# Performance work log

Hardware: AMD Instinct MI355X
Metric: run time of the kernel (lower is better)

The kernel has to match this reference:

```python
import jax, jax.numpy as jnp
import numpy as np
from jax import lax

D_STATE, D_ADAPT, D_CNN, D_RNN, D_OUT, HORIZON = 12, 16, 64, 256, 2, 10
B, L, H, W = 32, 16, 112, 112
DN = ('NCHW', 'OIHW', 'NCHW')
BN_EPS = 1e-5


def setup_inputs() -> dict:
    key = jax.random.key(0)
    ks = jax.random.split(key, 22)
    rn = lambda k, shape, s=0.05: jax.random.normal(k, shape, jnp.float32) * s
    return {
        'x': jax.random.normal(ks[0], (B, L, D_STATE), jnp.float32),
        'frames': jax.random.normal(ks[1], (B, L, 3, H, W), jnp.float32),
        # backbone `cnn`: 16x16 stride-16 patchify conv 3 -> 576 (gives 7x7 spatial)
        'cnn_w': rn(ks[2], (576, 3, 16, 16)), 'cnn_b': rn(ks[3], (576,)),
        # cnn_1: Conv2d(576, 64, 3, padding=1) + ReLU + BatchNorm (eval) + Dropout (eval=identity)
        'cnn1_w': rn(ks[4], (D_CNN, 576, 3, 3)), 'cnn1_b': rn(ks[5], (D_CNN,)),
        'bn_g': jnp.ones((D_CNN,), jnp.float32), 'bn_b': jnp.zeros((D_CNN,), jnp.float32),
        'bn_m': jnp.zeros((D_CNN,), jnp.float32), 'bn_v': jnp.ones((D_CNN,), jnp.float32),
        'a0_w': rn(ks[6], (D_ADAPT, D_STATE)), 'a0_b': rn(ks[7], (D_ADAPT,)),
        'ai_w': rn(ks[8], (D_ADAPT, D_ADAPT)), 'ai_b': rn(ks[9], (D_ADAPT,)),
        'an_w': rn(ks[10], (D_RNN, D_CNN + D_ADAPT)), 'an_b': rn(ks[11], (D_RNN,)),
        # single-layer batch_first GRU, PyTorch gate layout [r, z, n]
        'w_ih': rn(ks[12], (3 * D_RNN, D_RNN)), 'w_hh': rn(ks[13], (3 * D_RNN, D_RNN)),
        'b_ih': rn(ks[14], (3 * D_RNN,)), 'b_hh': rn(ks[15], (3 * D_RNN,)),
        'fi_w': rn(ks[16], (D_RNN, D_RNN)), 'fi_b': rn(ks[17], (D_RNN,)),
        'fn_w': rn(ks[18], (D_OUT, D_RNN)), 'fn_b': rn(ks[19], (D_OUT,)),
    }


def _gru_cell(xt, h, w_ih, w_hh, b_ih, b_hh):
    gi = xt @ w_ih.T + b_ih  # (B, 3*D)
    gh = h @ w_hh.T + b_hh
    i_r, i_z, i_n = jnp.split(gi, 3, axis=-1)
    h_r, h_z, h_n = jnp.split(gh, 3, axis=-1)
    r = jax.nn.sigmoid(i_r + h_r)
    z = jax.nn.sigmoid(i_z + h_z)
    n = jnp.tanh(i_n + r * h_n)
    return (1.0 - z) * n + z * h


def _forward(x, frames, cnn_w, cnn_b, cnn1_w, cnn1_b, bn_g, bn_b, bn_m, bn_v,
             a0_w, a0_b, ai_w, ai_b, an_w, an_b, w_ih, w_hh, b_ih, b_hh,
             fi_w, fi_b, fn_w, fn_b):
    b, l = frames.shape[0], frames.shape[1]
    f = frames.reshape((-1,) + frames.shape[-3:])  # (b*l, 3, H, W)
    # backbone cnn: patchify conv -> (b*l, 576, 7, 7)
    f = lax.conv_general_dilated(f, cnn_w, (16, 16), 'VALID', dimension_numbers=DN) + cnn_b[:, None, None]
    # cnn_1: Conv3x3 same -> ReLU -> BatchNorm(eval) -> Dropout(eval=identity)
    f = lax.conv_general_dilated(f, cnn1_w, (1, 1), 'SAME', dimension_numbers=DN) + cnn1_b[:, None, None]
    f = jax.nn.relu(f)
    inv = bn_g / jnp.sqrt(bn_v + BN_EPS)
    f = (f - bn_m[:, None, None]) * inv[:, None, None] + bn_b[:, None, None]
    # AdaptiveAvgPool2d((1,1)) then reshape to (b, l, d_cnn)
    f = f.mean(axis=(2, 3)).reshape(b, l, -1)
    # state adapters
    s = jax.nn.relu(x @ a0_w.T + a0_b)
    s = s + jax.nn.relu(s @ ai_w.T + ai_b)
    s = jnp.concatenate([s, f], axis=-1)  # (b, l, d_cnn + d_adapt)
    s = jax.nn.relu(s @ an_w.T + an_b)    # (b, l, d_rnn)
    # encoder GRU over the l frames
    d_rnn = w_hh.shape[1]
    h0 = jnp.zeros((b, d_rnn), s.dtype)
    def enc_step(h, xt):
        h2 = _gru_cell(xt, h, w_ih, w_hh, b_ih, b_hh)
        return h2, None
    h, _ = lax.scan(enc_step, h0, jnp.swapaxes(s, 0, 1))
    x_in = h  # last output of single-layer GRU == final hidden state
    def dec_step(carry, _):
        xi, hh = carry
        hn = _gru_cell(xi, hh, w_ih, w_hh, b_ih, b_hh)  # one GRU step; output == new hidden
        xr = hn + jax.nn.relu(hn @ fi_w.T + fi_b)       # final_i residual
        pred = jnp.tanh(xr @ fn_w.T + fn_b)             # final_n head
        return (xr, hn), pred
    _, preds = lax.scan(dec_step, (x_in, h), None, length=HORIZON)
    return preds[:, :, None, :]  # (horizon, b, 1, d_out) matching torch.stack of (b,1,d_out)


def reference(x, frames, cnn_w, cnn_b, cnn1_w, cnn1_b, bn_g, bn_b, bn_m, bn_v,
              a0_w, a0_b, ai_w, ai_b, an_w, an_b, w_ih, w_hh, b_ih, b_hh,
              fi_w, fi_b, fn_w, fn_b):
    return _forward(x, frames, cnn_w, cnn_b, cnn1_w, cnn1_b, bn_g, bn_b, bn_m, bn_v,
                    a0_w, a0_b, ai_w, ai_b, an_w, an_b, w_ih, w_hh, b_ih, b_hh,
                    fi_w, fi_b, fn_w, fn_b)
```

## Files before the change

kernel.cpp:

```cpp
#include <hip/hip_runtime.h>

typedef unsigned short u16;
typedef unsigned int u32;
typedef __bf16 bf16x8 __attribute__((ext_vector_type(8)));
typedef float f32x4 __attribute__((ext_vector_type(4)));
typedef unsigned short u16x8 __attribute__((ext_vector_type(8)));
typedef unsigned int u32x4 __attribute__((ext_vector_type(4)));
typedef _Float16 v2h __attribute__((ext_vector_type(2)));

__device__ __forceinline__ u16 f2bf(float f) {
    unsigned u = __float_as_uint(f);
    u = (u + 0x7fffu + ((u >> 16) & 1u)) >> 16;
    return (u16)u;
}
__device__ __forceinline__ float bf2f(u16 h) {
    return __uint_as_float((unsigned)h << 16);
}
__device__ __forceinline__ u32 packh2(float a, float b) {
    _Float16 ha = (_Float16)a, hb = (_Float16)b;
    u16 la = __builtin_bit_cast(u16, ha), lb = __builtin_bit_cast(u16, hb);
    return (u32)la | ((u32)lb << 16);
}
__device__ __forceinline__ float dot2acc(u32 w, u32 h, float acc) {
#if __has_builtin(__builtin_amdgcn_fdot2)
    return __builtin_amdgcn_fdot2(__builtin_bit_cast(v2h, w),
                                  __builtin_bit_cast(v2h, h), acc, false);
#else
    v2h wv = __builtin_bit_cast(v2h, w), hv = __builtin_bit_cast(v2h, h);
    return acc + (float)wv.x * (float)hv.x + (float)wv.y * (float)hv.y;
#endif
}
__device__ __forceinline__ float dot8(u32x4 w, u32x4 h, float acc) {
    acc = dot2acc(w.x, h.x, acc);
    acc = dot2acc(w.y, h.y, acc);
    acc = dot2acc(w.z, h.z, acc);
    acc = dot2acc(w.w, h.w, acc);
    return acc;
}
__device__ __forceinline__ void gload_lds16(const void* g, void* l) {
    __builtin_amdgcn_global_load_lds(
        (const __attribute__((address_space(1))) unsigned int*)g,
        (__attribute__((address_space(3))) unsigned int*)l, 16, 0, 0);
}

__global__ __launch_bounds__(256) void prep_kernel(
    const float* __restrict__ cnn_w, const float* __restrict__ cnn1_w,
    const float* __restrict__ w_hh, const float* __restrict__ w_ih,
    const float* __restrict__ fi_w,
    u16* __restrict__ B1, u16* __restrict__ B2,
    u32* __restrict__ whh8, u32* __restrict__ wih8, u32* __restrict__ fi8,
    u32* __restrict__ zpage)
{
    int idx = blockIdx.x * 256 + threadIdx.x;
    if (idx < 442368) { B1[idx] = f2bf(cnn_w[idx]); return; }
    idx -= 442368;
    if (idx < 331776) {
        int n = idx / 5184, rem = idx - n * 5184;
        int off = rem / 576, c = rem - off * 576;
        int dy = off / 3, dx = off - dy * 3;
        B2[idx] = f2bf(cnn1_w[((n * 576 + c) * 3 + dy) * 3 + dx]);
        return;
    }
    idx -= 331776;
    if (idx < 98304) {
        int kb = idx / 3072, r = idx - kb * 3072;
        int o = r >> 2, c = r & 3;
        int kk = kb * 8 + c * 2;
        whh8[idx] = packh2(w_hh[o * 256 + kk], w_hh[o * 256 + kk + 1]);
        return;
    }
    idx -= 98304;
    if (idx < 98304) {
        int kb = idx / 3072, r = idx - kb * 3072;
        int o = r >> 2, c = r & 3;
        int kk = kb * 8 + c * 2;
        wih8[idx] = packh2(w_ih[o * 256 + kk], w_ih[o * 256 + kk + 1]);
        return;
    }
    idx -= 98304;
    if (idx < 32768) {
        int kb = idx / 1024, r = idx - kb * 1024;
        int u = r >> 2, c = r & 3;
        int kk = kb * 8 + c * 2;
        fi8[idx] = packh2(fi_w[u * 256 + kk], fi_w[u * 256 + kk + 1]);
        return;
    }
    idx -= 32768;
    if (idx < 1024) zpage[idx] = 0u;
}

__global__ __launch_bounds__(256) void prep2_kernel(
    const float* __restrict__ w_ih, u16* __restrict__ wih_hi, u16* __restrict__ wih_lo)
{
    int idx = blockIdx.x * 256 + threadIdx.x;
    if (idx < 196608) {
        float v = w_ih[idx];
        u16 hi = f2bf(v);
        wih_hi[idx] = hi;
        wih_lo[idx] = f2bf(v - bf2f(hi));
    }
}

__global__ __launch_bounds__(256) void fconv_kernel(
    const float* __restrict__ frames, u16* __restrict__ fbf)
{
    size_t i = ((size_t)blockIdx.x * 256 + threadIdx.x) * 8;
    float4 a = *(const float4*)(frames + i);
    float4 b = *(const float4*)(frames + i + 4);
    u16x8 v = { f2bf(a.x), f2bf(a.y), f2bf(a.z), f2bf(a.w),
                f2bf(b.x), f2bf(b.y), f2bf(b.z), f2bf(b.w) };
    __builtin_nontemporal_store(v, (u16x8*)(fbf + i));
}

__global__ __launch_bounds__(256) void gemm1_v2(
    const u16* __restrict__ fbf, const u16* __restrict__ B1,
    const float* __restrict__ cnn_b, u16* __restrict__ f1)
{
    __shared__ u16 As[128 * 64];
    __shared__ u16 Bs[64 * 64];
    const int t = threadIdx.x, bx = blockIdx.x;
    const int m0 = (bx / 9) * 128, n0 = (bx % 9) * 64;
    const int wave = t >> 6, lane = t & 63;
    const int lm = lane & 15, lq = lane >> 4;

    f32x4 acc[2][4];
#pragma unroll
    for (int i = 0; i < 2; ++i)
#pragma unroll
        for (int q = 0; q < 4; ++q) acc[i][q] = (f32x4){0.f, 0.f, 0.f, 0.f};

    int ac8[4]; size_t abase[4];
#pragma unroll
    for (int i = 0; i < 4; ++i) {
        int s = wave * 256 + i * 64 + lane;
        int row = s >> 3, cc = s & 7;
        ac8[i] = cc ^ (row & 7);
        int m = m0 + row;
        int fr = m / 49, pos = m - fr * 49;
        int py = pos / 7, px = pos - py * 7;
        abase[i] = (size_t)fr * 37632 + py * 1792 + px * 16;
    }
    int bn[2], bc8[2];
#pragma unroll
    for (int i = 0; i < 2; ++i) {
        int s = wave * 128 + i * 64 + lane;
        int n = s >> 3, cc = s & 7;
        bn[i] = n; bc8[i] = cc ^ (n & 7);
    }

    for (int kt = 0; kt < 12; ++kt) {
        const int k0 = kt * 64;
#pragma unroll
        for (int i = 0; i < 4; ++i) {
            int k = k0 + ac8[i] * 8;
            int c = k >> 8, dy = (k >> 4) & 15, dx = k & 15;
            gload_lds16(fbf + abase[i] + c * 12544 + dy * 112 + dx,
                        &As[(wave * 256 + i * 64) * 8]);
        }
#pragma unroll
        for (int i = 0; i < 2; ++i) {
            gload_lds16(B1 + (size_t)(n0 + bn[i]) * 768 + k0 + bc8[i] * 8,
                        &Bs[(wave * 128 + i * 64) * 8]);
        }
        __syncthreads();
#pragma unroll
        for (int s = 0; s < 2; ++s) {
            bf16x8 a[2], b[4];
#pragma unroll
            for (int mi = 0; mi < 2; ++mi) {
                int row = wave * 32 + mi * 16 + lm;
                int c8 = s * 4 + lq;
                a[mi] = *(const bf16x8*)(&As[(row * 8 + (c8 ^ (row & 7))) * 8]);
            }
#pragma unroll
            for (int q = 0; q < 4; ++q) {
                int n = q * 16 + lm;
                int c8 = s * 4 + lq;
                b[q] = *(const bf16x8*)(&Bs[(n * 8 + (c8 ^ (n & 7))) * 8]);
            }
#pragma unroll
            for (int mi = 0; mi < 2; ++mi)
#pragma unroll
                for (int q = 0; q < 4; ++q)
                    acc[mi][q] = __builtin_amdgcn_mfma_f32_16x16x32_bf16(a[mi], b[q], acc[mi][q], 0, 0, 0);
        }
        __syncthreads();
    }
#pragma unroll
    for (int mi = 0; mi < 2; ++mi) {
#pragma unroll
        for (int q = 0; q < 4; ++q) {
            int n = n0 + q * 16 + lm;
            float bias = cnn_b[n];
#pragma unroll
            for (int r = 0; r < 4; ++r) {
                int m = m0 + wave * 32 + mi * 16 + lq * 4 + r;
                __builtin_nontemporal_store(f2bf(acc[mi][q][r] + bias), &f1[(size_t)m * 576 + n]);
            }
        }
    }
}

__global__ __launch_bounds__(256) void gemm1_patchify(
    const float* __restrict__ frames, const u16* __restrict__ B1,
    const float* __restrict__ cnn_b, u16* __restrict__ f1)
{
    __shared__ u16 As[128 * 64];
    __shared__ u16 Bs[64 * 64];
    const int t = threadIdx.x;
    const int bx = blockIdx.x;
    const int m0 = (bx / 9) * 128;
    const int n0 = (bx % 9) * 64;
    const int wave = t >> 6, lane = t & 63;
    const int lm = lane & 15, lq = lane >> 4;

    f32x4 acc[2][4];
#pragma unroll
    for (int i = 0; i < 2; ++i)
#pragma unroll
        for (int q = 0; q < 4; ++q) acc[i][q] = (f32x4){0.f, 0.f, 0.f, 0.f};

    int arow[4], ac8[4], abase[4];
#pragma unroll
    for (int i = 0; i < 4; ++i) {
        int cid = t + i * 256;
        int row = cid >> 3, c8 = cid & 7;
        int m = m0 + row;
        int fr = m / 49, pos = m - fr * 49;
        int py = pos / 7, px = pos - py * 7;
        arow[i] = row; ac8[i] = c8;
        abase[i] = (fr * 3 * 112 + py * 16) * 112 + px * 16;
    }

    for (int kt = 0; kt < 12; ++kt) {
        const int k0 = kt * 64;
#pragma unroll
        for (int i = 0; i < 4; ++i) {
            int k = k0 + ac8[i] * 8;
            int c = k >> 8, dy = (k >> 4) & 15, dx = k & 15;
            const float* src = frames + abase[i] + (c * 112 + dy) * 112 + dx;
            float4 v0 = *(const float4*)src;
            float4 v1 = *(const float4*)(src + 4);
            u16x8 v = { f2bf(v0.x), f2bf(v0.y), f2bf(v0.z), f2bf(v0.w),
                        f2bf(v1.x), f2bf(v1.y), f2bf(v1.z), f2bf(v1.w) };
            int sidx = arow[i] * 8 + (ac8[i] ^ (arow[i] & 7));
            *(u16x8*)(&As[sidx * 8]) = v;
        }
#pragma unroll
        for (int i = 0; i < 2; ++i) {
            int cid = t + i * 256;
            int n = cid >> 3, c8 = cid & 7;
            u16x8 v = *(const u16x8*)(B1 + (size_t)(n0 + n) * 768 + k0 + c8 * 8);
            int sidx = n * 8 + (c8 ^ (n & 7));
            *(u16x8*)(&Bs[sidx * 8]) = v;
        }
        __syncthreads();
#pragma unroll
        for (int s = 0; s < 2; ++s) {
            bf16x8 a[2], b[4];
#pragma unroll
            for (int mi = 0; mi < 2; ++mi) {
                int row = wave * 32 + mi * 16 + lm;
                int c8 = s * 4 + lq;
                a[mi] = *(const bf16x8*)(&As[(row * 8 + (c8 ^ (row & 7))) * 8]);
            }
#pragma unroll
            for (int q = 0; q < 4; ++q) {
                int n = q * 16 + lm;
                int c8 = s * 4 + lq;
                b[q] = *(const bf16x8*)(&Bs[(n * 8 + (c8 ^ (n & 7))) * 8]);
            }
#pragma unroll
            for (int mi = 0; mi < 2; ++mi)
#pragma unroll
                for (int q = 0; q < 4; ++q)
                    acc[mi][q] = __builtin_amdgcn_mfma_f32_16x16x32_bf16(a[mi], b[q], acc[mi][q], 0, 0, 0);
        }
        __syncthreads();
    }
#pragma unroll
    for (int mi = 0; mi < 2; ++mi) {
#pragma unroll
        for (int q = 0; q < 4; ++q) {
            int n = n0 + q * 16 + lm;
            float bias = cnn_b[n];
#pragma unroll
            for (int r = 0; r < 4; ++r) {
                int m = m0 + wave * 32 + mi * 16 + lq * 4 + r;
                __builtin_nontemporal_store(f2bf(acc[mi][q][r] + bias), &f1[(size_t)m * 576 + n]);
            }
        }
    }
}

__global__ __launch_bounds__(256) void gemm2_v2(
    const u16* __restrict__ f1, const u16* __restrict__ B2,
    const u16* __restrict__ zpage, float* __restrict__ C2)
{
    __shared__ u16 As[64 * 64];
    __shared__ u16 Bs[64 * 64];
    const int t = threadIdx.x;
    const int m0 = blockIdx.x * 64;
    const int wave = t >> 6, lane = t & 63;
    const int lm = lane & 15, lq = lane >> 4;

    f32x4 acc[4];
#pragma unroll
    for (int q = 0; q < 4; ++q) acc[q] = (f32x4){0.f, 0.f, 0.f, 0.f};

    int ac8[2], afr[2], apy[2], apx[2];
#pragma unroll
    for (int i = 0; i < 2; ++i) {
        int s = wave * 128 + i * 64 + lane;
        int row = s >> 3, cc = s & 7;
        ac8[i] = cc ^ (row & 7);
        int m = m0 + row;
        int fr = m / 49, pos = m - fr * 49;
        int py = pos / 7;
        afr[i] = fr; apy[i] = py; apx[i] = pos - py * 7;
    }
    int bn[2], bc8[2];
#pragma unroll
    for (int i = 0; i < 2; ++i) {
        int s = wave * 128 + i * 64 + lane;
        int n = s >> 3, cc = s & 7;
        bn[i] = n; bc8[i] = cc ^ (n & 7);
    }

    for (int kt = 0; kt < 81; ++kt) {
        int off = kt / 9, cb = kt - off * 9;
        int dy = off / 3, dx = off - dy * 3;
        int c0 = cb * 64;
#pragma unroll
        for (int i = 0; i < 2; ++i) {
            int yy = apy[i] + dy - 1, xx = apx[i] + dx - 1;
            const u16* g = ((unsigned)yy < 7u && (unsigned)xx < 7u)
                ? f1 + ((size_t)(afr[i] * 49 + yy * 7 + xx)) * 576 + c0 + ac8[i] * 8
                : zpage;
            gload_lds16(g, &As[(wave * 128 + i * 64) * 8]);
        }
#pragma unroll
        for (int i = 0; i < 2; ++i) {
            gload_lds16(B2 + (size_t)bn[i] * 5184 + kt * 64 + bc8[i] * 8,
                        &Bs[(wave * 128 + i * 64) * 8]);
        }
        __syncthreads();
#pragma unroll
        for (int s = 0; s < 2; ++s) {
            int row = wave * 16 + lm;
            int c8 = s * 4 + lq;
            bf16x8 a = *(const bf16x8*)(&As[(row * 8 + (c8 ^ (row & 7))) * 8]);
            bf16x8 b[4];
#pragma unroll
            for (int q = 0; q < 4; ++q) {
                int n = q * 16 + lm;
                b[q] = *(const bf16x8*)(&Bs[(n * 8 + (c8 ^ (n & 7))) * 8]);
            }
#pragma unroll
            for (int q = 0; q < 4; ++q)
                acc[q] = __builtin_amdgcn_mfma_f32_16x16x32_bf16(a, b[q], acc[q], 0, 0, 0);
        }
        __syncthreads();
    }
#pragma unroll
    for (int q = 0; q < 4; ++q)
#pragma unroll
        for (int r = 0; r < 4; ++r) {
            int m = m0 + wave * 16 + lq * 4 + r;
            int n = q * 16 + lm;
            __builtin_nontemporal_store(acc[q][r], &C2[(size_t)m * 64 + n]);
        }
}

__global__ __launch_bounds__(256) void reduce_kernel(
    const float* __restrict__ C2, const float* __restrict__ cnn1_b,
    const float* __restrict__ bn_g, const float* __restrict__ bn_b,
    const float* __restrict__ bn_m, const float* __restrict__ bn_v,
    float* __restrict__ fmean)
{
    int idx = blockIdx.x * 256 + threadIdx.x;
    int bl = idx >> 6, ch = idx & 63;
    float bias = cnn1_b[ch];
    const float* p = C2 + (size_t)bl * 49 * 64 + ch;
    float s = 0.f;
#pragma unroll
    for (int i = 0; i < 49; ++i) s += fmaxf(p[i * 64] + bias, 0.f);
    float mean = s * (1.f / 49.f);
    float inv = bn_g[ch] * rsqrtf(bn_v[ch] + 1e-5f);
    fmean[idx] = (mean - bn_m[ch]) * inv + bn_b[ch];
}

__global__ __launch_bounds__(256) void adapter_kernel(
    const float* __restrict__ x, const float* __restrict__ fmean,
    const float* __restrict__ a0_w, const float* __restrict__ a0_b,
    const float* __restrict__ ai_w, const float* __restrict__ ai_b,
    const float* __restrict__ an_w, const float* __restrict__ an_b,
    u16* __restrict__ zx_hi, u16* __restrict__ zx_lo)
{
    const int bl = blockIdx.x, t = threadIdx.x;
    __shared__ float s0[16];
    __shared__ float sf[80];
    if (t < 16) {
        float a = a0_b[t];
        const float* xp = x + bl * 12;
#pragma unroll
        for (int i = 0; i < 12; ++i) a += xp[i] * a0_w[t * 12 + i];
        s0[t] = fmaxf(a, 0.f);
    }
    __syncthreads();
    if (t < 16) {
        float a = ai_b[t];
#pragma unroll
        for (int i = 0; i < 16; ++i) a += s0[i] * ai_w[t * 16 + i];
        sf[t] = s0[t] + fmaxf(a, 0.f);
    } else if (t < 80) {
        sf[t] = fmean[bl * 64 + (t - 16)];
    }
    __syncthreads();
    float a = an_b[t];
#pragma unroll 8
    for (int i = 0; i < 80; ++i) a += sf[i] * an_w[t * 80 + i];
    a = fmaxf(a, 0.f);
    u16 hi = f2bf(a);
    zx_hi[bl * 256 + t] = hi;
    zx_lo[bl * 256 + t] = f2bf(a - bf2f(hi));
}

__global__ __launch_bounds__(256) void gi_kernel(
    const u16* __restrict__ zx_hi, const u16* __restrict__ zx_lo,
    const u16* __restrict__ wih_hi, const u16* __restrict__ wih_lo,
    const float* __restrict__ b_ih, float* __restrict__ gi_pre)
{
    __shared__ u16 Ah[128 * 64], Al[128 * 64];
    __shared__ u16 Bh[64 * 64], Bl[64 * 64];
    const int t = threadIdx.x, bx = blockIdx.x;
    const int m0 = (bx / 12) * 128, n0 = (bx % 12) * 64;
    const int wave = t >> 6, lane = t & 63;
    const int lm = lane & 15, lq = lane >> 4;

    f32x4 acc[2][4];
#pragma unroll
    for (int i = 0; i < 2; ++i)
#pragma unroll
        for (int q = 0; q < 4; ++q) acc[i][q] = (f32x4){0.f, 0.f, 0.f, 0.f};

    for (int kt = 0; kt < 4; ++kt) {
        const int k0 = kt * 64;
#pragma unroll
        for (int i = 0; i < 4; ++i) {
            int cid = t + i * 256;
            int row = cid >> 3, c8 = cid & 7;
            size_t src = (size_t)(m0 + row) * 256 + k0 + c8 * 8;
            int sidx = (row * 8 + (c8 ^ (row & 7))) * 8;
            *(u16x8*)(&Ah[sidx]) = *(const u16x8*)(zx_hi + src);
            *(u16x8*)(&Al[sidx]) = *(const u16x8*)(zx_lo + src);
        }
#pragma unroll
        for (int i = 0; i < 2; ++i) {
            int cid = t + i * 256;
            int n = cid >> 3, c8 = cid & 7;
            size_t src = (size_t)(n0 + n) * 256 + k0 + c8 * 8;
            int sidx = (n * 8 + (c8 ^ (n & 7))) * 8;
            *(u16x8*)(&Bh[sidx]) = *(const u16x8*)(wih_hi + src);
            *(u16x8*)(&Bl[sidx]) = *(const u16x8*)(wih_lo + src);
        }
        __syncthreads();
#pragma unroll
        for (int s = 0; s < 2; ++s) {
            bf16x8 ah[2], al[2], bh[4], blv[4];
#pragma unroll
            for (int mi = 0; mi < 2; ++mi) {
                int row = wave * 32 + mi * 16 + lm;
                int c8 = s * 4 + lq;
                int sidx = (row * 8 + (c8 ^ (row & 7))) * 8;
                ah[mi] = *(const bf16x8*)(&Ah[sidx]);
                al[mi] = *(const bf16x8*)(&Al[sidx]);
            }
#pragma unroll
            for (int q = 0; q < 4; ++q) {
                int n = q * 16 + lm;
                int c8 = s * 4 + lq;
                int sidx = (n * 8 + (c8 ^ (n & 7))) * 8;
                bh[q] = *(const bf16x8*)(&Bh[sidx]);
                blv[q] = *(const bf16x8*)(&Bl[sidx]);
            }
#pragma unroll
            for (int mi = 0; mi < 2; ++mi)
#pragma unroll
                for (int q = 0; q < 4; ++q) {
                    acc[mi][q] = __builtin_amdgcn_mfma_f32_16x16x32_bf16(ah[mi], bh[q], acc[mi][q], 0, 0, 0);
                    acc[mi][q] = __builtin_amdgcn_mfma_f32_16x16x32_bf16(ah[mi], blv[q], acc[mi][q], 0, 0, 0);
                    acc[mi][q] = __builtin_amdgcn_mfma_f32_16x16x32_bf16(al[mi], bh[q], acc[mi][q], 0, 0, 0);
                }
        }
        __syncthreads();
    }
#pragma unroll
    for (int q = 0; q < 4; ++q) {
        int n = n0 + q * 16 + lm;
        float bias = b_ih[n];
#pragma unroll
        for (int mi = 0; mi < 2; ++mi)
#pragma unroll
            for (int r = 0; r < 4; ++r) {
                int m = m0 + wave * 32 + mi * 16 + lq * 4 + r;
                gi_pre[(size_t)m * 768 + n] = acc[mi][q][r] + bias;
            }
    }
}

__global__ __launch_bounds__(768) void rnn_stream2(
    const float* __restrict__ gi_pre,
    const u32x4* __restrict__ whh8, const u32x4* __restrict__ wih8,
    const u32x4* __restrict__ fi8,
    const float* __restrict__ b_ih, const float* __restrict__ b_hh,
    const float* __restrict__ fi_b,
    const float* __restrict__ fn_w, const float* __restrict__ fn_b,
    float* __restrict__ out)
{
    extern __shared__ __align__(16) u32 slab[];
    const int b = blockIdx.x, t = threadIdx.x;
    const int wave = t >> 6;
    __shared__ __align__(16) u32 h2[128];
    __shared__ __align__(16) u32 x2[128];
    __shared__ float sA[768];
    __shared__ float sB[256];
    __shared__ float parts[768];
    __shared__ float pp[8];

#pragma unroll
    for (int j = 0; j < 12; ++j)
        *(u32x4*)&slab[(j * 768 + t) * 4] = whh8[j * 768 + t];

    const float bhh = b_hh[t];
    const float bih = b_ih[t];
    float hprev = 0.f;
    if (t < 128) h2[t] = 0u;
    __syncthreads();

    for (int l = 0; l < 16; ++l) {
        float gi = gi_pre[(size_t)(b * 16 + l) * 768 + t];
        float ah = 0.f;
#pragma unroll
        for (int j = 0; j < 12; ++j) {
            u32x4 w = *(const u32x4*)&slab[(j * 768 + t) * 4];
            u32x4 hh = *(const u32x4*)&h2[j * 4];
            ah = dot8(w, hh, ah);
        }
#pragma unroll 4
        for (int j = 0; j < 20; ++j) {
            int jj = j + wave; if (jj >= 20) jj -= 20;
            int kb = 12 + jj;
            u32x4 w = whh8[(size_t)kb * 768 + t];
            u32x4 hh = *(const u32x4*)&h2[kb * 4];
            ah = dot8(w, hh, ah);
        }
        if (t < 512) sA[t] = gi + ah + bhh;
        else { sA[t] = gi; sB[t - 512] = ah + bhh; }
        __syncthreads();
        if (t < 256) {
            float r = 1.f / (1.f + expf(-sA[t]));
            float z = 1.f / (1.f + expf(-sA[256 + t]));
            float n = tanhf(sA[512 + t] + r * sB[t]);
            hprev = (1.f - z) * n + z * hprev;
            float partner = __shfl_xor(hprev, 1);
            if ((t & 1) == 0) h2[t >> 1] = packh2(hprev, partner);
        }
        __syncthreads();
    }

    float xprev = hprev;
    if (t < 128) x2[t] = h2[t];
    __syncthreads();

    for (int d = 0; d < 10; ++d) {
        float ah = 0.f, ax = 0.f;
#pragma unroll
        for (int j = 0; j < 12; ++j) {
            u32x4 w = *(const u32x4*)&slab[(j * 768 + t) * 4];
            u32x4 hh = *(const u32x4*)&h2[j * 4];
            ah = dot8(w, hh, ah);
        }
#pragma unroll 4
        for (int j = 0; j < 20; ++j) {
            int jj = j + wave; if (jj >= 20) jj -= 20;
            int kb = 12 + jj;
            u32x4 w = whh8[(size_t)kb * 768 + t];
            u32x4 hh = *(const u32x4*)&h2[kb * 4];
            ah = dot8(w, hh, ah);
        }
#pragma unroll 4
        for (int j = 0; j < 32; ++j) {
            int jj = (j + wave * 3) & 31;
            u32x4 w = wih8[(size_t)jj * 768 + t];
            u32x4 xx = *(const u32x4*)&x2[jj * 4];
            ax = dot8(w, xx, ax);
        }
        if (t < 512) sA[t] = ax + bih + ah + bhh;
        else { sA[t] = ax + bih; sB[t - 512] = ah + bhh; }
        __syncthreads();
        if (t < 256) {
            float r = 1.f / (1.f + expf(-sA[t]));
            float z = 1.f / (1.f + expf(-sA[256 + t]));
            float n = tanhf(sA[512 + t] + r * sB[t]);
            hprev = (1.f - z) * n + z * hprev;
            float partner = __shfl_xor(hprev, 1);
            if ((t & 1) == 0) h2[t >> 1] = packh2(hprev, partner);
        }
        __syncthreads();
        {
            int u = t & 255, s = t >> 8;
            float afi = 0.f;
            for (int j = s; j < 32; j += 3) {
                u32x4 w = fi8[j * 256 + u];
                u32x4 hh = *(const u32x4*)&h2[j * 4];
                afi = dot8(w, hh, afi);
            }
            parts[t] = afi;
        }
        __syncthreads();
        if (t < 256) {
            float a = parts[t] + parts[256 + t] + parts[512 + t] + fi_b[t];
            xprev = hprev + fmaxf(a, 0.f);
            float partner = __shfl_xor(xprev, 1);
            if ((t & 1) == 0) x2[t >> 1] = packh2(xprev, partner);
            float c0 = xprev * fn_w[t];
            float c1 = xprev * fn_w[256 + t];
#pragma unroll
            for (int off = 32; off >= 1; off >>= 1) {
                c0 += __shfl_down(c0, off);
                c1 += __shfl_down(c1, off);
            }
            if ((t & 63) == 0) { pp[(t >> 6) * 2] = c0; pp[(t >> 6) * 2 + 1] = c1; }
        }
        __syncthreads();
        if (t < 2)
            out[d * 64 + b * 2 + t] =
                tanhf(fn_b[t] + pp[t] + pp[2 + t] + pp[4 + t] + pp[6 + t]);
    }
}

extern "C" void kernel_launch(void* const* d_in, const int* in_sizes, int n_in,
                              void* d_out, int out_size, void* d_ws, size_t ws_size,
                              hipStream_t stream)
{
    const float* x      = (const float*)d_in[0];
    const float* frames = (const float*)d_in[1];
    const float* cnn_w  = (const float*)d_in[2];
    const float* cnn_b  = (const float*)d_in[3];
    const float* cnn1_w = (const float*)d_in[4];
    const float* cnn1_b = (const float*)d_in[5];
    const float* bn_g   = (const float*)d_in[6];
    const float* bn_b   = (const float*)d_in[7];
    const float* bn_m   = (const float*)d_in[8];
    const float* bn_v   = (const float*)d_in[9];
    const float* a0_w   = (const float*)d_in[10];
    const float* a0_b   = (const float*)d_in[11];
    const float* ai_w   = (const float*)d_in[12];
    const float* ai_b   = (const float*)d_in[13];
    const float* an_w   = (const float*)d_in[14];
    const float* an_b   = (const float*)d_in[15];
    const float* w_ih   = (const float*)d_in[16];
    const float* w_hh   = (const float*)d_in[17];
    const float* b_ih   = (const float*)d_in[18];
    const float* b_hh   = (const float*)d_in[19];
    const float* fi_w   = (const float*)d_in[20];
    const float* fi_b   = (const float*)d_in[21];
    const float* fn_w   = (const float*)d_in[22];
    const float* fn_b   = (const float*)d_in[23];
    float* out = (float*)d_out;

    char* ws = (char*)d_ws;
    u16*   f1     = (u16*)(ws);
    u16*   B1     = (u16*)(ws + 28901376);
    u16*   B2     = (u16*)(ws + 29786112);
    float* C2     = (float*)(ws + 30449664);
    float* fmean  = (float*)(ws + 36872192);
    u32*   whh8   = (u32*)(ws + 37003264);
    u32*   wih8   = (u32*)(ws + 37396480);
    u32*   fi8    = (u32*)(ws + 37789696);
    u32*   zpage  = (u32*)(ws + 37920768);
    float* gi_pre = (float*)(ws + 30449664);
    u16*   wih_hi = (u16*)(ws + 32022528);
    u16*   wih_lo = (u16*)(ws + 32415744);
    u16*   zx_hi  = (u16*)(ws + 32808960);
    u16*   zx_lo  = (u16*)(ws + 33071104);
    u16*   fbf    = (u16*)(ws + 37924864);

    const bool big = ws_size >= 76460032ull;

    prep_kernel<<<3924, 256, 0, stream>>>(cnn_w, cnn1_w, w_hh, w_ih, fi_w,
                                          B1, B2, whh8, wih8, fi8, zpage);
    if (big) {
        fconv_kernel<<<9408, 256, 0, stream>>>(frames, fbf);
        gemm1_v2<<<196 * 9, 256, 0, stream>>>(fbf, B1, cnn_b, f1);
    } else {
        gemm1_patchify<<<196 * 9, 256, 0, stream>>>(frames, B1, cnn_b, f1);
    }
    gemm2_v2<<<392, 256, 0, stream>>>(f1, B2, (const u16*)zpage, C2);
    reduce_kernel<<<128, 256, 0, stream>>>(C2, cnn1_b, bn_g, bn_b, bn_m, bn_v, fmean);
    prep2_kernel<<<768, 256, 0, stream>>>(w_ih, wih_hi, wih_lo);
    adapter_kernel<<<512, 256, 0, stream>>>(x, fmean, a0_w, a0_b, ai_w, ai_b,
                                            an_w, an_b, zx_hi, zx_lo);
    gi_kernel<<<48, 256, 0, stream>>>(zx_hi, zx_lo, wih_hi, wih_lo, b_ih, gi_pre);
    hipFuncSetAttribute((const void*)rnn_stream2,
                        hipFuncAttributeMaxDynamicSharedMemorySize, 147456);
    rnn_stream2<<<32, 768, 147456, stream>>>(gi_pre, (const u32x4*)whh8,
                                             (const u32x4*)wih8, (const u32x4*)fi8,
                                             b_ih, b_hh, fi_b, fn_w, fn_b, out);
}
```

Before: 426.5 us.

## Fuse prep kernels, widen gemm1 N-tile, batch weight loads in GRU loops

Folds the frame bf16 conversion into prep_kernel and the w_ih hi/lo split into the adapter kernel, which removes two launches. gemm1 now computes a 128x192 tile per block instead of 128x64, so each A tile is reused across three times as many columns, at the cost of more accumulator registers and fewer blocks. The GRU recurrent loops issue all global weight loads into register arrays before the dot products and split each sum across two accumulators for more ILP. This raises register pressure in the 768-thread kernel.

```diff
diff --git a/kernel.cpp b/kernel.cpp
--- a/kernel.cpp
+++ b/kernel.cpp
@@ -46,11 +46,20 @@
 __global__ __launch_bounds__(256) void prep_kernel(
     const float* __restrict__ cnn_w, const float* __restrict__ cnn1_w,
     const float* __restrict__ w_hh, const float* __restrict__ w_ih,
-    const float* __restrict__ fi_w,
+    const float* __restrict__ fi_w, const float* __restrict__ frames,
     u16* __restrict__ B1, u16* __restrict__ B2,
     u32* __restrict__ whh8, u32* __restrict__ wih8, u32* __restrict__ fi8,
-    u32* __restrict__ zpage)
-{
+    u32* __restrict__ zpage, u16* __restrict__ fbf)
+{
+    if (blockIdx.x >= 3924) {
+        size_t i = ((size_t)(blockIdx.x - 3924) * 256 + threadIdx.x) * 8;
+        float4 a = *(const float4*)(frames + i);
+        float4 b = *(const float4*)(frames + i + 4);
+        u16x8 v = { f2bf(a.x), f2bf(a.y), f2bf(a.z), f2bf(a.w),
+                    f2bf(b.x), f2bf(b.y), f2bf(b.z), f2bf(b.w) };
+        __builtin_nontemporal_store(v, (u16x8*)(fbf + i));
+        return;
+    }
     int idx = blockIdx.x * 256 + threadIdx.x;
     if (idx < 442368) { B1[idx] = f2bf(cnn_w[idx]); return; }
     idx -= 442368;
@@ -89,45 +98,22 @@
     if (idx < 1024) zpage[idx] = 0u;
 }
 
-__global__ __launch_bounds__(256) void prep2_kernel(
-    const float* __restrict__ w_ih, u16* __restrict__ wih_hi, u16* __restrict__ wih_lo)
-{
-    int idx = blockIdx.x * 256 + threadIdx.x;
-    if (idx < 196608) {
-        float v = w_ih[idx];
-        u16 hi = f2bf(v);
-        wih_hi[idx] = hi;
-        wih_lo[idx] = f2bf(v - bf2f(hi));
-    }
-}
-
-__global__ __launch_bounds__(256) void fconv_kernel(
-    const float* __restrict__ frames, u16* __restrict__ fbf)
-{
-    size_t i = ((size_t)blockIdx.x * 256 + threadIdx.x) * 8;
-    float4 a = *(const float4*)(frames + i);
-    float4 b = *(const float4*)(frames + i + 4);
-    u16x8 v = { f2bf(a.x), f2bf(a.y), f2bf(a.z), f2bf(a.w),
-                f2bf(b.x), f2bf(b.y), f2bf(b.z), f2bf(b.w) };
-    __builtin_nontemporal_store(v, (u16x8*)(fbf + i));
-}
-
-__global__ __launch_bounds__(256) void gemm1_v2(
+__global__ __launch_bounds__(256) void gemm1_v3(
     const u16* __restrict__ fbf, const u16* __restrict__ B1,
     const float* __restrict__ cnn_b, u16* __restrict__ f1)
 {
     __shared__ u16 As[128 * 64];
-    __shared__ u16 Bs[64 * 64];
+    __shared__ u16 Bs[192 * 64];
     const int t = threadIdx.x, bx = blockIdx.x;
-    const int m0 = (bx / 9) * 128, n0 = (bx % 9) * 64;
+    const int m0 = (bx / 3) * 128, n0 = (bx % 3) * 192;
     const int wave = t >> 6, lane = t & 63;
     const int lm = lane & 15, lq = lane >> 4;
 
-    f32x4 acc[2][4];
+    f32x4 acc[2][12];
 #pragma unroll
     for (int i = 0; i < 2; ++i)
 #pragma unroll
-        for (int q = 0; q < 4; ++q) acc[i][q] = (f32x4){0.f, 0.f, 0.f, 0.f};
+        for (int q = 0; q < 12; ++q) acc[i][q] = (f32x4){0.f, 0.f, 0.f, 0.f};
 
     int ac8[4]; size_t abase[4];
 #pragma unroll
@@ -140,10 +126,10 @@
         int py = pos / 7, px = pos - py * 7;
         abase[i] = (size_t)fr * 37632 + py * 1792 + px * 16;
     }
-    int bn[2], bc8[2];
-#pragma unroll
-    for (int i = 0; i < 2; ++i) {
-        int s = wave * 128 + i * 64 + lane;
+    int bn[6], bc8[6];
+#pragma unroll
+    for (int i = 0; i < 6; ++i) {
+        int s = wave * 384 + i * 64 + lane;
         int n = s >> 3, cc = s & 7;
         bn[i] = n; bc8[i] = cc ^ (n & 7);
     }
@@ -158,38 +144,35 @@
                         &As[(wave * 256 + i * 64) * 8]);
         }
 #pragma unroll
-        for (int i = 0; i < 2; ++i) {
+        for (int i = 0; i < 6; ++i) {
             gload_lds16(B1 + (size_t)(n0 + bn[i]) * 768 + k0 + bc8[i] * 8,
-                        &Bs[(wave * 128 + i * 64) * 8]);
+                        &Bs[(wave * 384 + i * 64) * 8]);
         }
         __syncthreads();
 #pragma unroll
         for (int s = 0; s < 2; ++s) {
-            bf16x8 a[2], b[4];
+            int c8 = s * 4 + lq;
+            bf16x8 a[2];
 #pragma unroll
             for (int mi = 0; mi < 2; ++mi) {
                 int row = wave * 32 + mi * 16 + lm;
-                int c8 = s * 4 + lq;
                 a[mi] = *(const bf16x8*)(&As[(row * 8 + (c8 ^ (row & 7))) * 8]);
             }
 #pragma unroll
-            for (int q = 0; q < 4; ++q) {
+            for (int q = 0; q < 12; ++q) {
                 int n = q * 16 + lm;
-                int c8 = s * 4 + lq;
-                b[q] = *(const bf16x8*)(&Bs[(n * 8 + (c8 ^ (n & 7))) * 8]);
-            }
-#pragma unroll
-            for (int mi = 0; mi < 2; ++mi)
-#pragma unroll
-                for (int q = 0; q < 4; ++q)
-                    acc[mi][q] = __builtin_amdgcn_mfma_f32_16x16x32_bf16(a[mi], b[q], acc[mi][q], 0, 0, 0);
+                bf16x8 b = *(const bf16x8*)(&Bs[(n * 8 + (c8 ^ (n & 7))) * 8]);
+#pragma unroll
+                for (int mi = 0; mi < 2; ++mi)
+                    acc[mi][q] = __builtin_amdgcn_mfma_f32_16x16x32_bf16(a[mi], b, acc[mi][q], 0, 0, 0);
+            }
         }
         __syncthreads();
     }
 #pragma unroll
     for (int mi = 0; mi < 2; ++mi) {
 #pragma unroll
-        for (int q = 0; q < 4; ++q) {
+        for (int q = 0; q < 12; ++q) {
             int n = n0 + q * 16 + lm;
             float bias = cnn_b[n];
 #pragma unroll
@@ -390,14 +373,25 @@
     fmean[idx] = (mean - bn_m[ch]) * inv + bn_b[ch];
 }
 
-__global__ __launch_bounds__(256) void adapter_kernel(
+__global__ __launch_bounds__(256) void adapt_prep2_kernel(
     const float* __restrict__ x, const float* __restrict__ fmean,
     const float* __restrict__ a0_w, const float* __restrict__ a0_b,
     const float* __restrict__ ai_w, const float* __restrict__ ai_b,
     const float* __restrict__ an_w, const float* __restrict__ an_b,
-    u16* __restrict__ zx_hi, u16* __restrict__ zx_lo)
-{
-    const int bl = blockIdx.x, t = threadIdx.x;
+    const float* __restrict__ w_ih,
+    u16* __restrict__ zx_hi, u16* __restrict__ zx_lo,
+    u16* __restrict__ wih_hi, u16* __restrict__ wih_lo)
+{
+    const int t = threadIdx.x;
+    if (blockIdx.x >= 512) {
+        int idx = (blockIdx.x - 512) * 256 + t;
+        float v = w_ih[idx];
+        u16 hi = f2bf(v);
+        wih_hi[idx] = hi;
+        wih_lo[idx] = f2bf(v - bf2f(hi));
+        return;
+    }
+    const int bl = blockIdx.x;
     __shared__ float s0[16];
     __shared__ float sf[80];
     if (t < 16) {
@@ -509,7 +503,7 @@
     }
 }
 
-__global__ __launch_bounds__(768) void rnn_stream2(
+__global__ __launch_bounds__(768) void rnn_stream3(
     const float* __restrict__ gi_pre,
     const u32x4* __restrict__ whh8, const u32x4* __restrict__ wih8,
     const u32x4* __restrict__ fi8,
@@ -536,25 +530,34 @@
     const float bih = b_ih[t];
     float hprev = 0.f;
     if (t < 128) h2[t] = 0u;
+
+    int sjj[20];
+#pragma unroll
+    for (int j = 0; j < 20; ++j) {
+        int jj = j + wave; if (jj >= 20) jj -= 20;
+        sjj[j] = 12 + jj;
+    }
     __syncthreads();
 
     for (int l = 0; l < 16; ++l) {
         float gi = gi_pre[(size_t)(b * 16 + l) * 768 + t];
-        float ah = 0.f;
+        u32x4 w[20];
+#pragma unroll
+        for (int j = 0; j < 20; ++j)
+            w[j] = whh8[(size_t)sjj[j] * 768 + t];
+        float a0 = 0.f, a1 = 0.f;
 #pragma unroll
         for (int j = 0; j < 12; ++j) {
-            u32x4 w = *(const u32x4*)&slab[(j * 768 + t) * 4];
+            u32x4 ws = *(const u32x4*)&slab[(j * 768 + t) * 4];
             u32x4 hh = *(const u32x4*)&h2[j * 4];
-            ah = dot8(w, hh, ah);
-        }
-#pragma unroll 4
+            if (j & 1) a1 = dot8(ws, hh, a1); else a0 = dot8(ws, hh, a0);
+        }
+#pragma unroll
         for (int j = 0; j < 20; ++j) {
-            int jj = j + wave; if (jj >= 20) jj -= 20;
-            int kb = 12 + jj;
-            u32x4 w = whh8[(size_t)kb * 768 + t];
-            u32x4 hh = *(const u32x4*)&h2[kb * 4];
-            ah = dot8(w, hh, ah);
-        }
+            u32x4 hh = *(const u32x4*)&h2[sjj[j] * 4];
+            if (j & 1) a1 = dot8(w[j], hh, a1); else a0 = dot8(w[j], hh, a0);
+        }
+        float ah = a0 + a1;
         if (t < 512) sA[t] = gi + ah + bhh;
         else { sA[t] = gi; sB[t - 512] = ah + bhh; }
         __syncthreads();
@@ -574,28 +577,62 @@
     __syncthreads();
 
     for (int d = 0; d < 10; ++d) {
-        float ah = 0.f, ax = 0.f;
+        float a0 = 0.f, a1 = 0.f, x0 = 0.f, x1 = 0.f;
+        {
+            u32x4 w[10];
+#pragma unroll
+            for (int j = 0; j < 10; ++j) w[j] = whh8[(size_t)sjj[j] * 768 + t];
+#pragma unroll
+            for (int j = 0; j < 10; ++j) {
+                u32x4 hh = *(const u32x4*)&h2[sjj[j] * 4];
+                if (j & 1) a1 = dot8(w[j], hh, a1); else a0 = dot8(w[j], hh, a0);
+            }
+        }
+        {
+            u32x4 w[10];
+#pragma unroll
+            for (int j = 0; j < 10; ++j) w[j] = whh8[(size_t)sjj[10 + j] * 768 + t];
+#pragma unroll
+            for (int j = 0; j < 10; ++j) {
+                u32x4 hh = *(const u32x4*)&h2[sjj[10 + j] * 4];
+                if (j & 1) a1 = dot8(w[j], hh, a1); else a0 = dot8(w[j], hh, a0);
+            }
+        }
 #pragma unroll
         for (int j = 0; j < 12; ++j) {
-            u32x4 w = *(const u32x4*)&slab[(j * 768 + t) * 4];
+            u32x4 ws = *(const u32x4*)&slab[(j * 768 + t) * 4];
             u32x4 hh = *(const u32x4*)&h2[j * 4];
-            ah = dot8(w, hh, ah);
-        }
-#pragma unroll 4
-        for (int j = 0; j < 20; ++j) {
-            int jj = j + wave; if (jj >= 20) jj -= 20;
-            int kb = 12 + jj;
-            u32x4 w = whh8[(size_t)kb * 768 + t];
-            u32x4 hh = *(const u32x4*)&h2[kb * 4];
-            ah = dot8(w, hh, ah);
-        }
-#pragma unroll 4
-        for (int j = 0; j < 32; ++j) {
-            int jj = (j + wave * 3) & 31;
-            u32x4 w = wih8[(size_t)jj * 768 + t];
-            u32x4 xx = *(const u32x4*)&x2[jj * 4];
-            ax = dot8(w, xx, ax);
-        }
+            if (j & 1) a1 = dot8(ws, hh, a1); else a0 = dot8(ws, hh, a0);
+        }
+        {
+            u32x4 w[16];
+#pragma unroll
+            for (int j = 0; j < 16; ++j) {
+                int jj = (j + wave * 3) & 31;
+                w[j] = wih8[(size_t)jj * 768 + t];
+            }
+#pragma unroll
+            for (int j = 0; j < 16; ++j) {
+                int jj = (j + wave * 3) & 31;
+                u32x4 xx = *(const u32x4*)&x2[jj * 4];
+                if (j & 1) x1 = dot8(w[j], xx, x1); else x0 = dot8(w[j], xx, x0);
+            }
+        }
+        {
+            u32x4 w[16];
+#pragma unroll
+            for (int j = 0; j < 16; ++j) {
+                int jj = (16 + j + wave * 3) & 31;
+                w[j] = wih8[(size_t)jj * 768 + t];
+            }
+#pragma unroll
+            for (int j = 0; j < 16; ++j) {
+                int jj = (16 + j + wave * 3) & 31;
+                u32x4 xx = *(const u32x4*)&x2[jj * 4];
+                if (j & 1) x1 = dot8(w[j], xx, x1); else x0 = dot8(w[j], xx, x0);
+            }
+        }
+        float ah = a0 + a1, ax = x0 + x1;
         if (t < 512) sA[t] = ax + bih + ah + bhh;
         else { sA[t] = ax + bih; sB[t - 512] = ah + bhh; }
         __syncthreads();
@@ -610,13 +647,20 @@
         __syncthreads();
         {
             int u = t & 255, s = t >> 8;
-            float afi = 0.f;
-            for (int j = s; j < 32; j += 3) {
-                u32x4 w = fi8[j * 256 + u];
-                u32x4 hh = *(const u32x4*)&h2[j * 4];
-                afi = dot8(w, hh, afi);
-            }
-            parts[t] = afi;
+            u32x4 w[11];
+            int cnt = 0;
+#pragma unroll
+            for (int j = 0; j < 11; ++j) {
+                int jj = s + j * 3;
+                if (jj < 32) { w[j] = fi8[jj * 256 + u]; cnt = j + 1; }
+            }
+            float f0 = 0.f, f1v = 0.f;
+            for (int j = 0; j < cnt; ++j) {
+                int jj = s + j * 3;
+                u32x4 hh = *(const u32x4*)&h2[jj * 4];
+                if (j & 1) f1v = dot8(w[j], hh, f1v); else f0 = dot8(w[j], hh, f0);
+            }
+            parts[t] = f0 + f1v;
         }
         __syncthreads();
         if (t < 256) {
@@ -689,23 +733,23 @@
 
     const bool big = ws_size >= 76460032ull;
 
-    prep_kernel<<<3924, 256, 0, stream>>>(cnn_w, cnn1_w, w_hh, w_ih, fi_w,
-                                          B1, B2, whh8, wih8, fi8, zpage);
+    prep_kernel<<<big ? 13332 : 3924, 256, 0, stream>>>(
+        cnn_w, cnn1_w, w_hh, w_ih, fi_w, frames,
+        B1, B2, whh8, wih8, fi8, zpage, fbf);
     if (big) {
-        fconv_kernel<<<9408, 256, 0, stream>>>(frames, fbf);
-        gemm1_v2<<<196 * 9, 256, 0, stream>>>(fbf, B1, cnn_b, f1);
+        gemm1_v3<<<196 * 3, 256, 0, stream>>>(fbf, B1, cnn_b, f1);
     } else {
         gemm1_patchify<<<196 * 9, 256, 0, stream>>>(frames, B1, cnn_b, f1);
     }
     gemm2_v2<<<392, 256, 0, stream>>>(f1, B2, (const u16*)zpage, C2);
     reduce_kernel<<<128, 256, 0, stream>>>(C2, cnn1_b, bn_g, bn_b, bn_m, bn_v, fmean);
-    prep2_kernel<<<768, 256, 0, stream>>>(w_ih, wih_hi, wih_lo);
-    adapter_kernel<<<512, 256, 0, stream>>>(x, fmean, a0_w, a0_b, ai_w, ai_b,
-                                            an_w, an_b, zx_hi, zx_lo);
+    adapt_prep2_kernel<<<1280, 256, 0, stream>>>(x, fmean, a0_w, a0_b, ai_w, ai_b,
+                                                 an_w, an_b, w_ih,
+                                                 zx_hi, zx_lo, wih_hi, wih_lo);
     gi_kernel<<<48, 256, 0, stream>>>(zx_hi, zx_lo, wih_hi, wih_lo, b_ih, gi_pre);
-    hipFuncSetAttribute((const void*)rnn_stream2,
+    hipFuncSetAttribute((const void*)rnn_stream3,
                         hipFuncAttributeMaxDynamicSharedMemorySize, 147456);
-    rnn_stream2<<<32, 768, 147456, stream>>>(gi_pre, (const u32x4*)whh8,
+    rnn_stream3<<<32, 768, 147456, stream>>>(gi_pre, (const u32x4*)whh8,
                                              (const u32x4*)wih8, (const u32x4*)fi8,
                                              b_ih, b_hh, fi_b, fn_w, fn_b, out);
 }
```

Result: slower. 648.1 us (+51.9%).
